# Kernel optimization log

Measured on AMD Instinct MI355X. Metric: run time of the kernel, lower is better.

## Reference

```python
import jax, jax.numpy as jnp
import numpy as np

B, T, D = 2, 2048, 1024
H, HS = 16, 64  # n_head, head_size; H*HS == D
THETA = 10000.0


def setup_inputs() -> dict:
    key = jax.random.key(0)
    ks = jax.random.split(key, 10)
    s = 0.02
    return {
        "x": jax.random.normal(ks[0], (B, T, D), jnp.float32),
        "attention_mask": jnp.ones((B, T), jnp.int32),
        # weights stored [in, out] (transposed torch Linear weight)
        "Wq": jax.random.normal(ks[1], (D, H * HS), jnp.float32) * s,
        "bq": jax.random.normal(ks[2], (H * HS,), jnp.float32) * s,
        "Wk": jax.random.normal(ks[3], (D, H * HS), jnp.float32) * s,
        "bk": jax.random.normal(ks[4], (H * HS,), jnp.float32) * s,
        "Wv": jax.random.normal(ks[5], (D, H * HS), jnp.float32) * s,
        "bv": jax.random.normal(ks[6], (H * HS,), jnp.float32) * s,
        "Wo": jax.random.normal(ks[7], (H * HS, D), jnp.float32) * s,
        "bo": jax.random.normal(ks[8], (D,), jnp.float32) * s,
    }


def _rotate_half(x):
    x1, x2 = x[..., : HS // 2], x[..., HS // 2:]
    return jnp.concatenate((-x2, x1), axis=-1)


def _rope_tables(seq_len, dtype):
    inv_freq = 1.0 / (THETA ** (jnp.arange(0, HS, 2, dtype=jnp.float32) / HS))
    t = jnp.arange(seq_len, dtype=jnp.float32)
    freqs = t[:, None] * inv_freq[None, :]            # [T, HS/2]
    emb = jnp.concatenate((freqs, freqs), axis=-1)    # [T, HS]
    return jnp.cos(emb).astype(dtype), jnp.sin(emb).astype(dtype)


def attention_fwd(x, attention_mask, Wq, bq, Wk, bk, Wv, bv, Wo, bo):
    b, t, c = x.shape
    # QKV projections -> [B, H, T, HS]
    q = (x @ Wq + bq).reshape(b, t, H, HS).transpose(0, 2, 1, 3)
    k = (x @ Wk + bk).reshape(b, t, H, HS).transpose(0, 2, 1, 3)
    v = (x @ Wv + bv).reshape(b, t, H, HS).transpose(0, 2, 1, 3)
    # rotary embedding
    cos, sin = _rope_tables(t, x.dtype)               # [T, HS]
    q = q * cos + _rotate_half(q) * sin
    k = k * cos + _rotate_half(k) * sin
    # expanded causal+padding mask: mask[:,None,None,:] expanded to [B,1,T,T] then tril
    causal = jnp.tril(jnp.ones((t, t), dtype=bool))
    keep = (attention_mask[:, None, None, :] != 0) & causal[None, None]  # [B,1,T,T]
    scale = 1.0 / np.sqrt(HS)
    scores = jnp.einsum('bhqd,bhkd->bhqk', q, k) * scale
    scores = jnp.where(keep, scores, jnp.finfo(scores.dtype).min)
    att = jax.nn.softmax(scores, axis=-1)
    y = jnp.einsum('bhqk,bhkd->bhqd', att, v)         # [B,H,T,HS]
    y = y.transpose(0, 2, 1, 3).reshape(b, t, H * HS)
    return y @ Wo + bo


def reference(x, attention_mask, Wq, bq, Wk, bk, Wv, bv, Wo, bo):
    return attention_fwd(x, attention_mask, Wq, bq, Wk, bk, Wv, bv, Wo, bo)
```

## Files before the change

kernel.cpp:

```cpp
#include <hip/hip_runtime.h>

#define T_SEQ 2048
#define NB 2
#define NH 16
#define HS 64
#define DMODEL 1024
#define NEG_BIG (-3.0e38f)

typedef __attribute__((ext_vector_type(8))) short bf16x8;
typedef __attribute__((ext_vector_type(4))) float f32x4;
#define MFMA16 __builtin_amdgcn_mfma_f32_16x16x32_bf16

__device__ __forceinline__ unsigned short f2bfu(float f) {
    union { float f; unsigned int i; } z; z.f = f;
    unsigned int x = z.i;
    unsigned int r = x + 0x7fffu + ((x >> 16) & 1u);
    return (unsigned short)(r >> 16);
}
__device__ __forceinline__ unsigned int pack_bf16(float a, float b) {
    union { float f; unsigned int u; } x, y; x.f = a; y.f = b;
    return __builtin_amdgcn_perm(y.u + 0x8000u, x.u + 0x8000u, 0x07060302u);
}

__device__ __forceinline__ void gl2lds16(const unsigned short* g, unsigned short* l) {
    __builtin_amdgcn_global_load_lds(
        (const __attribute__((address_space(1))) unsigned int*)g,
        (__attribute__((address_space(3))) unsigned int*)l, 16, 0, 0);
}

__global__ __launch_bounds__(256) void convert_x_kernel(
    const float4* __restrict__ x4, ushort4* __restrict__ o4, int n4)
{
    int i = blockIdx.x * 256 + threadIdx.x;
    int stride = gridDim.x * 256;
    for (; i < n4; i += stride) {
        float4 f = x4[i];
        ushort4 u;
        u.x = f2bfu(f.x); u.y = f2bfu(f.y); u.z = f2bfu(f.z); u.w = f2bfu(f.w);
        o4[i] = u;
    }
}

__global__ __launch_bounds__(256) void transpose_w_kernel(
    const float* __restrict__ W0, const float* __restrict__ W1,
    const float* __restrict__ W2, const float* __restrict__ W3,
    unsigned short* __restrict__ T0, unsigned short* __restrict__ T1,
    unsigned short* __restrict__ T2, unsigned short* __restrict__ T3)
{
    __shared__ float tile[32][33];
    const float* W = (blockIdx.z == 0) ? W0 : (blockIdx.z == 1) ? W1 : (blockIdx.z == 2) ? W2 : W3;
    unsigned short* T = (blockIdx.z == 0) ? T0 : (blockIdx.z == 1) ? T1 : (blockIdx.z == 2) ? T2 : T3;
    const int k0 = blockIdx.x * 32, n0 = blockIdx.y * 32;
    const int t = threadIdx.x;
    const int r = t >> 5, c = t & 31;
    #pragma unroll
    for (int i = 0; i < 4; ++i)
        tile[r + 8 * i][c] = W[(size_t)(k0 + r + 8 * i) * DMODEL + n0 + c];
    __syncthreads();
    #pragma unroll
    for (int i = 0; i < 4; ++i)
        T[(size_t)(n0 + r + 8 * i) * DMODEL + k0 + c] = f2bfu(tile[c][r + 8 * i]);
}

__global__ __launch_bounds__(256) void qkv_mfma_kernel(
    const unsigned short* __restrict__ A,
    const unsigned short* __restrict__ Wqt, const unsigned short* __restrict__ Wkt,
    const unsigned short* __restrict__ Wvt,
    const float* __restrict__ bq, const float* __restrict__ bk, const float* __restrict__ bv,
    unsigned short* __restrict__ qo, unsigned short* __restrict__ ko,
    unsigned short* __restrict__ vt)
{
    __shared__ unsigned short As[128 * 32];
    __shared__ unsigned short Bs[128 * 32];
    const int tid = threadIdx.x;
    const int wave = tid >> 6, lane = tid & 63;
    const int lane15 = lane & 15, quad = lane >> 4;
    const int z = blockIdx.z;
    const unsigned short* Bt = (z == 0) ? Wqt : (z == 1) ? Wkt : Wvt;
    const float* bias = (z == 0) ? bq : (z == 1) ? bk : bv;
    const int m0 = blockIdx.x * 128, n0 = blockIdx.y * 128;
    const int mh = (wave & 1) * 64, nh = (wave >> 1) * 64;

    f32x4 acc[4][4];
    #pragma unroll
    for (int i = 0; i < 4; ++i)
        #pragma unroll
        for (int j = 0; j < 4; ++j) acc[i][j] = (f32x4){0.f, 0.f, 0.f, 0.f};

    const int c0 = tid, c1 = tid + 256;
    const int r0 = c0 >> 2, o0 = (c0 & 3) * 8;
    const int r1 = c1 >> 2, o1 = (c1 & 3) * 8;

    for (int kk = 0; kk < 32; ++kk) {
        __syncthreads();
        gl2lds16(A  + (size_t)(m0 + r0) * DMODEL + kk * 32 + o0, As + c0 * 8);
        gl2lds16(A  + (size_t)(m0 + r1) * DMODEL + kk * 32 + o1, As + c1 * 8);
        gl2lds16(Bt + (size_t)(n0 + r0) * DMODEL + kk * 32 + o0, Bs + c0 * 8);
        gl2lds16(Bt + (size_t)(n0 + r1) * DMODEL + kk * 32 + o1, Bs + c1 * 8);
        __syncthreads();
        bf16x8 af[4], bfr[4];
        #pragma unroll
        for (int i = 0; i < 4; ++i)
            af[i] = *(const bf16x8*)(As + (mh + i * 16 + lane15) * 32 + quad * 8);
        #pragma unroll
        for (int j = 0; j < 4; ++j)
            bfr[j] = *(const bf16x8*)(Bs + (nh + j * 16 + lane15) * 32 + quad * 8);
        #pragma unroll
        for (int i = 0; i < 4; ++i)
            #pragma unroll
            for (int j = 0; j < 4; ++j)
                acc[i][j] = MFMA16(af[i], bfr[j], acc[i][j], 0, 0, 0);
    }

    const int n0c = n0 + nh;
    const int head = n0c >> 6;
    const float bj0 = bias[n0c + lane15];
    const float bj1 = bias[n0c + 16 + lane15];
    const float bj2 = bias[n0c + 32 + lane15];
    const float bj3 = bias[n0c + 48 + lane15];

    if (z < 2) {
        unsigned short* outp = (z == 0) ? qo : ko;
        const float osc = (z == 0) ? 0.18033688011112042f : 1.0f;
        const float inv0 = __builtin_exp2f(-(float)(lane15)      * 0.41524101186092029f);
        const float inv1 = __builtin_exp2f(-(float)(lane15 + 16) * 0.41524101186092029f);
        #pragma unroll
        for (int i = 0; i < 4; ++i) {
            #pragma unroll
            for (int r = 0; r < 4; ++r) {
                int tok = m0 + mh + i * 16 + quad * 4 + r;
                int bb = tok >> 11, t = tok & (T_SEQ - 1);
                float a0 = (float)t * inv0, a1 = (float)t * inv1;
                float sn0, cs0, sn1, cs1;
                __sincosf(a0, &sn0, &cs0);
                __sincosf(a1, &sn1, &cs1);
                float v0 = acc[i][0][r] + bj0, v1 = acc[i][1][r] + bj1;
                float v2 = acc[i][2][r] + bj2, v3 = acc[i][3][r] + bj3;
                size_t base = ((size_t)(bb * NH + head) * T_SEQ + t) * HS;
                outp[base + lane15]      = f2bfu((v0 * cs0 - v2 * sn0) * osc);
                outp[base + 16 + lane15] = f2bfu((v1 * cs1 - v3 * sn1) * osc);
                outp[base + 32 + lane15] = f2bfu((v2 * cs0 + v0 * sn0) * osc);
                outp[base + 48 + lane15] = f2bfu((v3 * cs1 + v1 * sn1) * osc);
            }
        }
    } else {
        #pragma unroll
        for (int i = 0; i < 4; ++i) {
            int tok0_ = m0 + mh + i * 16 + quad * 4;
            int bb = tok0_ >> 11, t0 = tok0_ & (T_SEQ - 1);
            #pragma unroll
            for (int j = 0; j < 4; ++j) {
                float bj = (j == 0) ? bj0 : (j == 1) ? bj1 : (j == 2) ? bj2 : bj3;
                ushort4 u;
                u.x = f2bfu(acc[i][j][0] + bj);
                u.y = f2bfu(acc[i][j][1] + bj);
                u.z = f2bfu(acc[i][j][2] + bj);
                u.w = f2bfu(acc[i][j][3] + bj);
                *(ushort4*)(vt + ((size_t)(bb * NH + head) * HS + j * 16 + lane15) * T_SEQ + t0) = u;
            }
        }
    }
}

__global__ __launch_bounds__(128, 2) void attn_mfma_kernel(
    const unsigned short* __restrict__ q,
    const unsigned short* __restrict__ k,
    const unsigned short* __restrict__ vt,
    const int* __restrict__ mask,
    unsigned short* __restrict__ y)
{
    __shared__ unsigned short Ks[64 * 72];
    __shared__ unsigned short Vs[64 * 72];
    __shared__ unsigned short Pt[2][32 * 72];
    const int tid = threadIdx.x;
    const int wave = tid >> 6, lane = tid & 63;
    const int lane15 = lane & 15, quad = lane >> 4;
    const int bid = blockIdx.x;
    const int bh = bid & 31;
    const int qB = 31 - (bid >> 5);
    const int b = bh >> 4, h = bh & 15;
    const int q0 = qB * 64 + wave * 32;

    const unsigned short* kbase = k  + (size_t)bh * T_SEQ * HS;
    const unsigned short* vbase = vt + (size_t)bh * HS * T_SEQ;

    bf16x8 qf[2][2];
    #pragma unroll
    for (int g = 0; g < 2; ++g) {
        const unsigned short* qrow = q + ((size_t)bh * T_SEQ + q0 + g * 16 + lane15) * HS;
        qf[g][0] = *(const bf16x8*)(qrow + quad * 8);
        qf[g][1] = *(const bf16x8*)(qrow + 32 + quad * 8);
    }

    f32x4 accO[2][4];
    #pragma unroll
    for (int g = 0; g < 2; ++g)
        #pragma unroll
        for (int dt = 0; dt < 4; ++dt) accO[g][dt] = (f32x4){0.f, 0.f, 0.f, 0.f};
    float m_i[2] = {NEG_BIG, NEG_BIG}, l_i[2] = {0.f, 0.f};

    for (int kt = 0; kt <= qB; ++kt) {
        const int k0 = kt * 64;
        __syncthreads();
        #pragma unroll
        for (int it = 0; it < 4; ++it) {
            int cc = it * 128 + tid;
            int row = cc >> 3, off = (cc & 7) * 8;
            *(uint4*)(Ks + row * 72 + off) = *(const uint4*)(kbase + (size_t)(k0 + row) * HS + off);
            *(uint4*)(Vs + row * 72 + off) = *(const uint4*)(vbase + (size_t)row * T_SEQ + k0 + off);
        }
        unsigned long long bal = __ballot(mask[b * T_SEQ + k0 + lane] != 0);
        __syncthreads();

        f32x4 s[2][4];
        #pragma unroll
        for (int jt = 0; jt < 4; ++jt) {
            bf16x8 kf0 = *(const bf16x8*)(Ks + (jt * 16 + lane15) * 72 + quad * 8);
            bf16x8 kf1 = *(const bf16x8*)(Ks + (jt * 16 + lane15) * 72 + 32 + quad * 8);
            #pragma unroll
            for (int g = 0; g < 2; ++g) {
                f32x4 t_ = (f32x4){0.f, 0.f, 0.f, 0.f};
                t_ = MFMA16(kf0, qf[g][0], t_, 0, 0, 0);
                t_ = MFMA16(kf1, qf[g][1], t_, 0, 0, 0);
                s[g][jt] = t_;
            }
        }

        const bool need_mask = (k0 + 63 > q0) || (bal != ~0ull);
        float alpha_g[2];
        #pragma unroll
        for (int g = 0; g < 2; ++g) {
            const int qpos = q0 + g * 16 + lane15;
            if (need_mask) {
                #pragma unroll
                for (int jt = 0; jt < 4; ++jt) {
                    unsigned int mnib = (unsigned int)(bal >> (jt * 16 + quad * 4)) & 15u;
                    #pragma unroll
                    for (int r = 0; r < 4; ++r) {
                        int kpos = k0 + jt * 16 + quad * 4 + r;
                        bool ok = (kpos <= qpos) && ((mnib >> r) & 1u);
                        s[g][jt][r] = ok ? s[g][jt][r] : NEG_BIG;
                    }
                }
            }
            float mx = NEG_BIG;
            #pragma unroll
            for (int jt = 0; jt < 4; ++jt)
                #pragma unroll
                for (int r = 0; r < 4; ++r)
                    mx = fmaxf(mx, s[g][jt][r]);
            mx = fmaxf(mx, __shfl_xor(mx, 16));
            mx = fmaxf(mx, __shfl_xor(mx, 32));
            float mn = fmaxf(m_i[g], mx);
            alpha_g[g] = exp2f(m_i[g] - mn);
            m_i[g] = mn;
            float rs = 0.f;
            #pragma unroll
            for (int jt = 0; jt < 4; ++jt)
                #pragma unroll
                for (int r = 0; r < 4; ++r) {
                    float p = exp2f(s[g][jt][r] - mn);
                    s[g][jt][r] = p;
                    rs += p;
                }
            rs += __shfl_xor(rs, 16);
            rs += __shfl_xor(rs, 32);
            l_i[g] = l_i[g] * alpha_g[g] + rs;
        }

        #pragma unroll
        for (int g = 0; g < 2; ++g)
            #pragma unroll
            for (int jt = 0; jt < 4; ++jt) {
                unsigned int p01 = pack_bf16(s[g][jt][0], s[g][jt][1]);
                unsigned int p23 = pack_bf16(s[g][jt][2], s[g][jt][3]);
                *(uint2*)(&Pt[wave][(g * 16 + lane15) * 72 + jt * 16 + quad * 4]) = make_uint2(p01, p23);
            }

        float alr[2][4];
        #pragma unroll
        for (int g = 0; g < 2; ++g)
            #pragma unroll
            for (int r = 0; r < 4; ++r)
                alr[g][r] = __shfl(alpha_g[g], quad * 4 + r);
        #pragma unroll
        for (int g = 0; g < 2; ++g)
            #pragma unroll
            for (int dt = 0; dt < 4; ++dt)
                #pragma unroll
                for (int r = 0; r < 4; ++r)
                    accO[g][dt][r] *= alr[g][r];

        bf16x8 pf[2][2];
        #pragma unroll
        for (int g = 0; g < 2; ++g) {
            pf[g][0] = *(const bf16x8*)(&Pt[wave][(g * 16 + lane15) * 72 + quad * 8]);
            pf[g][1] = *(const bf16x8*)(&Pt[wave][(g * 16 + lane15) * 72 + 32 + quad * 8]);
        }
        #pragma unroll
        for (int dt = 0; dt < 4; ++dt) {
            bf16x8 vf0 = *(const bf16x8*)(Vs + (dt * 16 + lane15) * 72 + quad * 8);
            bf16x8 vf1 = *(const bf16x8*)(Vs + (dt * 16 + lane15) * 72 + 32 + quad * 8);
            #pragma unroll
            for (int g = 0; g < 2; ++g) {
                accO[g][dt] = MFMA16(pf[g][0], vf0, accO[g][dt], 0, 0, 0);
                accO[g][dt] = MFMA16(pf[g][1], vf1, accO[g][dt], 0, 0, 0);
            }
        }
    }

    float invr[2][4];
    #pragma unroll
    for (int g = 0; g < 2; ++g) {
        float invl = 1.0f / l_i[g];
        #pragma unroll
        for (int r = 0; r < 4; ++r)
            invr[g][r] = __shfl(invl, quad * 4 + r);
    }
    #pragma unroll
    for (int g = 0; g < 2; ++g)
        #pragma unroll
        for (int r = 0; r < 4; ++r) {
            int qpos = q0 + g * 16 + quad * 4 + r;
            unsigned short* yrow = y + (size_t)(b * T_SEQ + qpos) * DMODEL + h * HS;
            #pragma unroll
            for (int dt = 0; dt < 4; ++dt)
                yrow[dt * 16 + lane15] = f2bfu(accO[g][dt][r] * invr[g][r]);
        }
}

__global__ __launch_bounds__(256) void outproj_mfma_kernel(
    const unsigned short* __restrict__ A,
    const unsigned short* __restrict__ Bt,
    const float* __restrict__ bo, float* __restrict__ out)
{
    __shared__ unsigned short As[128 * 32];
    __shared__ unsigned short Bs[128 * 32];
    const int tid = threadIdx.x;
    const int wave = tid >> 6, lane = tid & 63;
    const int lane15 = lane & 15, quad = lane >> 4;
    const int m0 = blockIdx.x * 128, n0 = blockIdx.y * 128;
    const int mh = (wave & 1) * 64, nh = (wave >> 1) * 64;

    f32x4 acc[4][4];
    #pragma unroll
    for (int i = 0; i < 4; ++i)
        #pragma unroll
        for (int j = 0; j < 4; ++j) acc[i][j] = (f32x4){0.f, 0.f, 0.f, 0.f};

    const int c0 = tid, c1 = tid + 256;
    const int r0 = c0 >> 2, o0 = (c0 & 3) * 8;
    const int r1 = c1 >> 2, o1 = (c1 & 3) * 8;

    for (int kk = 0; kk < 32; ++kk) {
        __syncthreads();
        gl2lds16(A  + (size_t)(m0 + r0) * DMODEL + kk * 32 + o0, As + c0 * 8);
        gl2lds16(A  + (size_t)(m0 + r1) * DMODEL + kk * 32 + o1, As + c1 * 8);
        gl2lds16(Bt + (size_t)(n0 + r0) * DMODEL + kk * 32 + o0, Bs + c0 * 8);
        gl2lds16(Bt + (size_t)(n0 + r1) * DMODEL + kk * 32 + o1, Bs + c1 * 8);
        __syncthreads();
        bf16x8 af[4], bfr[4];
        #pragma unroll
        for (int i = 0; i < 4; ++i)
            af[i] = *(const bf16x8*)(As + (mh + i * 16 + lane15) * 32 + quad * 8);
        #pragma unroll
        for (int j = 0; j < 4; ++j)
            bfr[j] = *(const bf16x8*)(Bs + (nh + j * 16 + lane15) * 32 + quad * 8);
        #pragma unroll
        for (int i = 0; i < 4; ++i)
            #pragma unroll
            for (int j = 0; j < 4; ++j)
                acc[i][j] = MFMA16(af[i], bfr[j], acc[i][j], 0, 0, 0);
    }

    const int n0c = n0 + nh;
    const float bj0 = bo[n0c + lane15];
    const float bj1 = bo[n0c + 16 + lane15];
    const float bj2 = bo[n0c + 32 + lane15];
    const float bj3 = bo[n0c + 48 + lane15];
    #pragma unroll
    for (int i = 0; i < 4; ++i) {
        #pragma unroll
        for (int r = 0; r < 4; ++r) {
            int tok = m0 + mh + i * 16 + quad * 4 + r;
            float* orow = out + (size_t)tok * DMODEL + n0c;
            orow[lane15]      = acc[i][0][r] + bj0;
            orow[16 + lane15] = acc[i][1][r] + bj1;
            orow[32 + lane15] = acc[i][2][r] + bj2;
            orow[48 + lane15] = acc[i][3][r] + bj3;
        }
    }
}

extern "C" void kernel_launch(void* const* d_in, const int* in_sizes, int n_in,
                              void* d_out, int out_size, void* d_ws, size_t ws_size,
                              hipStream_t stream)
{
    const float* x  = (const float*)d_in[0];
    const int* mask = (const int*)d_in[1];
    const float* Wq = (const float*)d_in[2];
    const float* bq = (const float*)d_in[3];
    const float* Wk = (const float*)d_in[4];
    const float* bk = (const float*)d_in[5];
    const float* Wv = (const float*)d_in[6];
    const float* bv = (const float*)d_in[7];
    const float* Wo = (const float*)d_in[8];
    const float* bo = (const float*)d_in[9];

    unsigned short* ws = (unsigned short*)d_ws;
    const size_t M1 = 1024 * 1024;
    unsigned short* xb  = ws;
    unsigned short* Wqt = ws + 4 * M1;
    unsigned short* Wkt = ws + 5 * M1;
    unsigned short* Wvt = ws + 6 * M1;
    unsigned short* Wot = ws + 7 * M1;
    unsigned short* qw  = ws + 8 * M1;
    unsigned short* kw  = ws + 12 * M1;
    unsigned short* vtw = ws + 16 * M1;
    unsigned short* yw  = ws + 20 * M1;

    convert_x_kernel<<<1024, 256, 0, stream>>>(
        (const float4*)x, (ushort4*)xb, (NB * T_SEQ * DMODEL) / 4);
    transpose_w_kernel<<<dim3(32, 32, 4), 256, 0, stream>>>(
        Wq, Wk, Wv, Wo, Wqt, Wkt, Wvt, Wot);
    qkv_mfma_kernel<<<dim3(32, 8, 3), 256, 0, stream>>>(
        xb, Wqt, Wkt, Wvt, bq, bk, bv, qw, kw, vtw);
    attn_mfma_kernel<<<1024, 128, 0, stream>>>(
        qw, kw, vtw, mask, yw);
    outproj_mfma_kernel<<<dim3(32, 8), 256, 0, stream>>>(
        yw, Wot, bo, (float*)d_out);
}
```

Measured before the change: 226.7 us.

## Split long causal attention rows into KV chunks, merge prep kernels, shrink outproj tile

Query blocks past index 16 now process their key range in two chunks of up to 16 tiles. Each chunk writes unnormalized partial outputs plus running max and sum, and a new combine kernel merges them flash-decoding style. This evens out per-block work and raises the attention block count. The x-convert and weight-transpose kernels are merged into one launch to save a launch. The output projection uses 64-row M tiles for more blocks. In exchange it adds an extra kernel, an extra round trip of partials through bf16 which may cost accuracy, and extra launch overhead.

```diff
diff --git a/kernel.cpp b/kernel.cpp
--- a/kernel.cpp
+++ b/kernel.cpp
@@ -11,6 +11,9 @@
 typedef __attribute__((ext_vector_type(4))) float f32x4;
 #define MFMA16 __builtin_amdgcn_mfma_f32_16x16x32_bf16
 
+__device__ __forceinline__ float bfu2f(unsigned int u) {
+    union { unsigned int i; float f; } z; z.i = u << 16; return z.f;
+}
 __device__ __forceinline__ unsigned short f2bfu(float f) {
     union { float f; unsigned int i; } z; z.f = f;
     unsigned int x = z.i;
@@ -28,38 +31,36 @@
         (__attribute__((address_space(3))) unsigned int*)l, 16, 0, 0);
 }
 
-__global__ __launch_bounds__(256) void convert_x_kernel(
-    const float4* __restrict__ x4, ushort4* __restrict__ o4, int n4)
-{
-    int i = blockIdx.x * 256 + threadIdx.x;
-    int stride = gridDim.x * 256;
-    for (; i < n4; i += stride) {
-        float4 f = x4[i];
-        ushort4 u;
-        u.x = f2bfu(f.x); u.y = f2bfu(f.y); u.z = f2bfu(f.z); u.w = f2bfu(f.w);
-        o4[i] = u;
-    }
-}
-
-__global__ __launch_bounds__(256) void transpose_w_kernel(
+__global__ __launch_bounds__(256) void prep_kernel(
+    const float4* __restrict__ x4, ushort4* __restrict__ o4,
     const float* __restrict__ W0, const float* __restrict__ W1,
     const float* __restrict__ W2, const float* __restrict__ W3,
     unsigned short* __restrict__ T0, unsigned short* __restrict__ T1,
     unsigned short* __restrict__ T2, unsigned short* __restrict__ T3)
 {
-    __shared__ float tile[32][33];
-    const float* W = (blockIdx.z == 0) ? W0 : (blockIdx.z == 1) ? W1 : (blockIdx.z == 2) ? W2 : W3;
-    unsigned short* T = (blockIdx.z == 0) ? T0 : (blockIdx.z == 1) ? T1 : (blockIdx.z == 2) ? T2 : T3;
-    const int k0 = blockIdx.x * 32, n0 = blockIdx.y * 32;
     const int t = threadIdx.x;
-    const int r = t >> 5, c = t & 31;
-    #pragma unroll
-    for (int i = 0; i < 4; ++i)
-        tile[r + 8 * i][c] = W[(size_t)(k0 + r + 8 * i) * DMODEL + n0 + c];
-    __syncthreads();
-    #pragma unroll
-    for (int i = 0; i < 4; ++i)
-        T[(size_t)(n0 + r + 8 * i) * DMODEL + k0 + c] = f2bfu(tile[c][r + 8 * i]);
+    if (blockIdx.z < 4) {
+        __shared__ float tile[32][33];
+        const float* W = (blockIdx.z == 0) ? W0 : (blockIdx.z == 1) ? W1 : (blockIdx.z == 2) ? W2 : W3;
+        unsigned short* T = (blockIdx.z == 0) ? T0 : (blockIdx.z == 1) ? T1 : (blockIdx.z == 2) ? T2 : T3;
+        const int k0 = blockIdx.x * 32, n0 = blockIdx.y * 32;
+        const int r = t >> 5, c = t & 31;
+        #pragma unroll
+        for (int i = 0; i < 4; ++i)
+            tile[r + 8 * i][c] = W[(size_t)(k0 + r + 8 * i) * DMODEL + n0 + c];
+        __syncthreads();
+        #pragma unroll
+        for (int i = 0; i < 4; ++i)
+            T[(size_t)(n0 + r + 8 * i) * DMODEL + k0 + c] = f2bfu(tile[c][r + 8 * i]);
+    } else {
+        const int n4 = NB * T_SEQ * DMODEL / 4;
+        for (int i = (blockIdx.y * 32 + blockIdx.x) * 256 + t; i < n4; i += 32 * 32 * 256) {
+            float4 f = x4[i];
+            ushort4 u;
+            u.x = f2bfu(f.x); u.y = f2bfu(f.y); u.z = f2bfu(f.z); u.w = f2bfu(f.w);
+            o4[i] = u;
+        }
+    }
 }
 
 __global__ __launch_bounds__(256) void qkv_mfma_kernel(
@@ -167,7 +168,8 @@
     const unsigned short* __restrict__ k,
     const unsigned short* __restrict__ vt,
     const int* __restrict__ mask,
-    unsigned short* __restrict__ y)
+    unsigned short* __restrict__ pO,
+    float* __restrict__ pml)
 {
     __shared__ unsigned short Ks[64 * 72];
     __shared__ unsigned short Vs[64 * 72];
@@ -177,9 +179,14 @@
     const int lane15 = lane & 15, quad = lane >> 4;
     const int bid = blockIdx.x;
     const int bh = bid & 31;
-    const int qB = 31 - (bid >> 5);
-    const int b = bh >> 4, h = bh & 15;
+    const int cid = 47 - (bid >> 5);
+    int qB, c;
+    if (cid < 16) { qB = cid; c = 0; }
+    else { int t = cid - 16; qB = 16 + (t >> 1); c = t & 1; }
+    const int slot = bh * 48 + ((qB < 16) ? qB : 16 + ((qB - 16) << 1)) + c;
+    const int b = bh >> 4;
     const int q0 = qB * 64 + wave * 32;
+    const int kt0 = c * 16, kt1 = (kt0 + 15 < qB) ? kt0 + 15 : qB;
 
     const unsigned short* kbase = k  + (size_t)bh * T_SEQ * HS;
     const unsigned short* vbase = vt + (size_t)bh * HS * T_SEQ;
@@ -199,7 +206,7 @@
         for (int dt = 0; dt < 4; ++dt) accO[g][dt] = (f32x4){0.f, 0.f, 0.f, 0.f};
     float m_i[2] = {NEG_BIG, NEG_BIG}, l_i[2] = {0.f, 0.f};
 
-    for (int kt = 0; kt <= qB; ++kt) {
+    for (int kt = kt0; kt <= kt1; ++kt) {
         const int k0 = kt * 64;
         __syncthreads();
         #pragma unroll
@@ -309,24 +316,65 @@
         }
     }
 
-    float invr[2][4];
-    #pragma unroll
-    for (int g = 0; g < 2; ++g) {
-        float invl = 1.0f / l_i[g];
-        #pragma unroll
-        for (int r = 0; r < 4; ++r)
-            invr[g][r] = __shfl(invl, quad * 4 + r);
-    }
+    unsigned short* ob = pO + (size_t)slot * 4096;
     #pragma unroll
     for (int g = 0; g < 2; ++g)
         #pragma unroll
         for (int r = 0; r < 4; ++r) {
-            int qpos = q0 + g * 16 + quad * 4 + r;
-            unsigned short* yrow = y + (size_t)(b * T_SEQ + qpos) * DMODEL + h * HS;
+            int row = wave * 32 + g * 16 + quad * 4 + r;
             #pragma unroll
             for (int dt = 0; dt < 4; ++dt)
-                yrow[dt * 16 + lane15] = f2bfu(accO[g][dt][r] * invr[g][r]);
-        }
+                ob[row * 64 + dt * 16 + lane15] = f2bfu(accO[g][dt][r]);
+        }
+    if (quad == 0) {
+        #pragma unroll
+        for (int g = 0; g < 2; ++g) {
+            int row = wave * 32 + g * 16 + lane15;
+            pml[slot * 128 + row]      = m_i[g];
+            pml[slot * 128 + 64 + row] = l_i[g];
+        }
+    }
+}
+
+__global__ __launch_bounds__(256) void attn_combine_kernel(
+    const unsigned short* __restrict__ pO, const float* __restrict__ pml,
+    unsigned short* __restrict__ y)
+{
+    const int qB = blockIdx.x, bh = blockIdx.y;
+    const int b = bh >> 4, h = bh & 15;
+    const int tid = threadIdx.x;
+    const int row = tid >> 2, cb = (tid & 3) * 16;
+    const int nch = (qB < 16) ? 1 : 2;
+    const int slot0 = bh * 48 + ((qB < 16) ? qB : 16 + ((qB - 16) << 1));
+    const float m0 = pml[slot0 * 128 + row];
+    const float l0 = pml[slot0 * 128 + 64 + row];
+    float w0 = 1.f, w1 = 0.f, L = l0;
+    if (nch == 2) {
+        float m1 = pml[(slot0 + 1) * 128 + row];
+        float l1 = pml[(slot0 + 1) * 128 + 64 + row];
+        float M = fmaxf(m0, m1);
+        w0 = exp2f(m0 - M); w1 = exp2f(m1 - M);
+        L = w0 * l0 + w1 * l1;
+    }
+    const float invL = 1.0f / L;
+    const unsigned short* o0 = pO + (size_t)slot0 * 4096 + row * 64 + cb;
+    const unsigned short* o1 = o0 + 4096;
+    unsigned short* yrow = y + (size_t)(b * T_SEQ + qB * 64 + row) * DMODEL + h * HS + cb;
+    #pragma unroll
+    for (int j = 0; j < 4; ++j) {
+        ushort4 u0 = *(const ushort4*)(o0 + j * 4);
+        float a0 = w0 * bfu2f(u0.x), a1 = w0 * bfu2f(u0.y);
+        float a2 = w0 * bfu2f(u0.z), a3 = w0 * bfu2f(u0.w);
+        if (nch == 2) {
+            ushort4 u1 = *(const ushort4*)(o1 + j * 4);
+            a0 += w1 * bfu2f(u1.x); a1 += w1 * bfu2f(u1.y);
+            a2 += w1 * bfu2f(u1.z); a3 += w1 * bfu2f(u1.w);
+        }
+        ushort4 o;
+        o.x = f2bfu(a0 * invL); o.y = f2bfu(a1 * invL);
+        o.z = f2bfu(a2 * invL); o.w = f2bfu(a3 * invL);
+        *(ushort4*)(yrow + j * 4) = o;
+    }
 }
 
 __global__ __launch_bounds__(256) void outproj_mfma_kernel(
@@ -334,40 +382,40 @@
     const unsigned short* __restrict__ Bt,
     const float* __restrict__ bo, float* __restrict__ out)
 {
-    __shared__ unsigned short As[128 * 32];
+    __shared__ unsigned short As[64 * 32];
     __shared__ unsigned short Bs[128 * 32];
     const int tid = threadIdx.x;
     const int wave = tid >> 6, lane = tid & 63;
     const int lane15 = lane & 15, quad = lane >> 4;
-    const int m0 = blockIdx.x * 128, n0 = blockIdx.y * 128;
-    const int mh = (wave & 1) * 64, nh = (wave >> 1) * 64;
-
-    f32x4 acc[4][4];
-    #pragma unroll
-    for (int i = 0; i < 4; ++i)
+    const int m0 = blockIdx.x * 64, n0 = blockIdx.y * 128;
+    const int mh = (wave & 1) * 32, nh = (wave >> 1) * 64;
+
+    f32x4 acc[2][4];
+    #pragma unroll
+    for (int i = 0; i < 2; ++i)
         #pragma unroll
         for (int j = 0; j < 4; ++j) acc[i][j] = (f32x4){0.f, 0.f, 0.f, 0.f};
 
+    const int ra = tid >> 2, oa = (tid & 3) * 8;
     const int c0 = tid, c1 = tid + 256;
     const int r0 = c0 >> 2, o0 = (c0 & 3) * 8;
     const int r1 = c1 >> 2, o1 = (c1 & 3) * 8;
 
     for (int kk = 0; kk < 32; ++kk) {
         __syncthreads();
-        gl2lds16(A  + (size_t)(m0 + r0) * DMODEL + kk * 32 + o0, As + c0 * 8);
-        gl2lds16(A  + (size_t)(m0 + r1) * DMODEL + kk * 32 + o1, As + c1 * 8);
+        gl2lds16(A  + (size_t)(m0 + ra) * DMODEL + kk * 32 + oa, As + tid * 8);
         gl2lds16(Bt + (size_t)(n0 + r0) * DMODEL + kk * 32 + o0, Bs + c0 * 8);
         gl2lds16(Bt + (size_t)(n0 + r1) * DMODEL + kk * 32 + o1, Bs + c1 * 8);
         __syncthreads();
-        bf16x8 af[4], bfr[4];
-        #pragma unroll
-        for (int i = 0; i < 4; ++i)
+        bf16x8 af[2], bfr[4];
+        #pragma unroll
+        for (int i = 0; i < 2; ++i)
             af[i] = *(const bf16x8*)(As + (mh + i * 16 + lane15) * 32 + quad * 8);
         #pragma unroll
         for (int j = 0; j < 4; ++j)
             bfr[j] = *(const bf16x8*)(Bs + (nh + j * 16 + lane15) * 32 + quad * 8);
         #pragma unroll
-        for (int i = 0; i < 4; ++i)
+        for (int i = 0; i < 2; ++i)
             #pragma unroll
             for (int j = 0; j < 4; ++j)
                 acc[i][j] = MFMA16(af[i], bfr[j], acc[i][j], 0, 0, 0);
@@ -379,7 +427,7 @@
     const float bj2 = bo[n0c + 32 + lane15];
     const float bj3 = bo[n0c + 48 + lane15];
     #pragma unroll
-    for (int i = 0; i < 4; ++i) {
+    for (int i = 0; i < 2; ++i) {
         #pragma unroll
         for (int r = 0; r < 4; ++r) {
             int tok = m0 + mh + i * 16 + quad * 4 + r;
@@ -418,15 +466,17 @@
     unsigned short* kw  = ws + 12 * M1;
     unsigned short* vtw = ws + 16 * M1;
     unsigned short* yw  = ws + 20 * M1;
-
-    convert_x_kernel<<<1024, 256, 0, stream>>>(
-        (const float4*)x, (ushort4*)xb, (NB * T_SEQ * DMODEL) / 4);
-    transpose_w_kernel<<<dim3(32, 32, 4), 256, 0, stream>>>(
-        Wq, Wk, Wv, Wo, Wqt, Wkt, Wvt, Wot);
+    unsigned short* pO  = ws + 24 * M1;
+    float* pml = (float*)(ws + 30 * M1);
+
+    prep_kernel<<<dim3(32, 32, 5), 256, 0, stream>>>(
+        (const float4*)x, (ushort4*)xb, Wq, Wk, Wv, Wo, Wqt, Wkt, Wvt, Wot);
     qkv_mfma_kernel<<<dim3(32, 8, 3), 256, 0, stream>>>(
         xb, Wqt, Wkt, Wvt, bq, bk, bv, qw, kw, vtw);
-    attn_mfma_kernel<<<1024, 128, 0, stream>>>(
-        qw, kw, vtw, mask, yw);
-    outproj_mfma_kernel<<<dim3(32, 8), 256, 0, stream>>>(
+    attn_mfma_kernel<<<1536, 128, 0, stream>>>(
+        qw, kw, vtw, mask, pO, pml);
+    attn_combine_kernel<<<dim3(32, 32), 256, 0, stream>>>(
+        pO, pml, yw);
+    outproj_mfma_kernel<<<dim3(64, 8), 256, 0, stream>>>(
         yw, Wot, bo, (float*)d_out);
 }
```

New measurement: 217.9 us. -3.9%, faster.
